# Kernel optimization log

Measured on AMD Instinct MI355X. Metric: run time of the kernel, lower is better.

Reference implementation:

```python
import jax, jax.numpy as jnp
import numpy as np

NINP, NHID, NOUT = 400, 600, 400
HS = NHID + NOUT          # h_size = nhid + nout
NLEVELS, K, AUX_FREQ = 40, 2, 20
DILATION = [1]


def setup_inputs() -> dict:
    key = jax.random.key(0)
    ks = jax.random.split(key, 6)
    B, T = 8, 256
    bound = 0.01  # matches init_weights normal_(0, 0.01)
    return {
        "X": jax.random.normal(ks[0], (B, NINP, T), jnp.float32),
        "hid": jax.random.normal(ks[1], (B, HS, 1), jnp.float32),
        "cell": jax.random.normal(ks[2], (B, HS, 1), jnp.float32),
        "w1": jax.random.normal(ks[3], (4 * HS, NINP, K), jnp.float32) * bound,
        "w2": jax.random.normal(ks[4], (4 * HS, HS, K), jnp.float32) * bound,
        "b2": jax.random.normal(ks[5], (4 * HS,), jnp.float32) * bound,
    }


def _conv1d(x, w, d):
    # x: [B, Cin, T_padded], w: [Cout, Cin, K] -> [B, Cout, T]
    return jax.lax.conv_general_dilated(
        x, w, window_strides=(1,), padding='VALID', rhs_dilation=(d,),
        dimension_numbers=('NCH', 'OIH', 'NCH'))


def _forward(X, hid, cell, w1, w2, b2):
    B, _, T = X.shape
    ht = jnp.zeros((B, HS, T), X.dtype)
    ct = jnp.zeros((B, HS, T), X.dtype)

    # Input-side convolution is weight-tied and X never changes across levels,
    # so (like the torch dict cache) compute it once per distinct dilation.
    conv1 = {}
    for d in set(DILATION):
        pad = (K - 1) * d
        xp = jnp.pad(X, ((0, 0), (0, 0), (pad, 0)))
        conv1[d] = _conv1d(xp, w1, d)

    aux = []
    for i in range(NLEVELS):
        d = DILATION[i % len(DILATION)]
        pad = (K - 1) * d
        # causal left-pad of the hidden stream, filled with the initial hid
        z1 = jnp.concatenate([jnp.broadcast_to(hid, (B, HS, pad)), ht], axis=2)
        out = conv1[d] + _conv1d(z1, w2, d) + b2[None, :, None]  # [B, 4*HS, T]
        # shifted cell state, first d steps filled with the initial cell
        ct_1 = jnp.concatenate(
            [jnp.broadcast_to(cell, (B, HS, d)), ct[:, :, :-d]], axis=2)
        it = jax.nn.sigmoid(out[:, :HS])
        ot = jax.nn.sigmoid(out[:, HS:2 * HS])
        gt = jnp.tanh(out[:, 2 * HS:3 * HS])
        ft = jax.nn.sigmoid(out[:, 3 * HS:])
        ct = ft * ct_1 + it * gt
        ht = ot * jnp.tanh(ct)
        if i % AUX_FREQ == AUX_FREQ - 1:
            aux.append(ht[:, -NOUT:])  # [B, nout, T]

    out_main = jnp.transpose(ht[:, -NOUT:], (0, 2, 1))            # [B, T, nout]
    hc = (ht[:, :, -1:], ct[:, :, -1:])                            # ([B,HS,1], [B,HS,1])
    aux_outs = jnp.transpose(jnp.stack(aux, axis=0), (1, 0, 3, 2))  # [B, n_aux, T, nout]
    return out_main, hc, aux_outs


def reference(X, hid, cell, w1, w2, b2):
    return _forward(X, hid, cell, w1, w2, b2)
```

## Files before the change

### kernel.cpp

```cpp
#include <hip/hip_runtime.h>
#include <hip/hip_bf16.h>
#include <math.h>

typedef __bf16 bf16;
typedef __bf16 bf16x8 __attribute__((ext_vector_type(8)));
typedef __bf16 bf16x4 __attribute__((ext_vector_type(4)));
typedef float f32x4 __attribute__((ext_vector_type(4)));
typedef float f32x16 __attribute__((ext_vector_type(16)));
typedef unsigned int u32;
typedef u32 u32x4 __attribute__((ext_vector_type(4)));

#define NINP 400
#define HS   1000
#define HP   1024
#define B_   8
#define T_   256
#define NT   2048
#define K2   2048
#define K1   1024
#define M_   4096

#define HT_OFF   819200
#define CT_OFF   827200
#define AUX_OFF  835200

typedef __attribute__((address_space(1))) const void gvoid;
typedef __attribute__((address_space(3))) void lvoid;

__device__ __forceinline__ void async_copy16(void* lds, const void* g) {
  __builtin_amdgcn_global_load_lds((gvoid*)g, (lvoid*)lds, 16, 0, 0);
}

__device__ __forceinline__ float sigm(float x) { return 1.0f / (1.0f + expf(-x)); }


__global__ void repack_w1(const float* __restrict__ w1, bf16* __restrict__ W1q) {
  int idx = blockIdx.x * 256 + threadIdx.x;
  if (idx >= M_ * K1) return;
  int m = idx >> 10, k = idx & 1023;
  int g = (m >> 3) & 3, h = (m >> 5) * 8 + (m & 7);
  float v = 0.0f;
  if (h < HS) {
    int c = g * HS + h;
    if (k < 512) { if (k < NINP) v = w1[(size_t)c * (NINP * 2) + k * 2 + 0]; }
    else { int j = k - 512; if (j < NINP) v = w1[(size_t)c * (NINP * 2) + j * 2 + 1]; }
  }
  W1q[idx] = (bf16)v;
}

__global__ void repack_w2(const float* __restrict__ w2, bf16* __restrict__ W2q) {
  int idx = blockIdx.x * 256 + threadIdx.x;
  if (idx >= M_ * K2) return;
  int m = idx >> 11, k = idx & 2047;
  int g = (m >> 3) & 3, h = (m >> 5) * 8 + (m & 7);
  float v = 0.0f;
  if (h < HS) {
    int c = g * HS + h;
    if (k < HP) { if (k < HS) v = w2[(size_t)c * (HS * 2) + k * 2 + 0]; }
    else { int j = k - HP; if (j < HS) v = w2[(size_t)c * (HS * 2) + j * 2 + 1]; }
  }
  W2q[idx] = (bf16)v;
}

__global__ void build_xt(const float* __restrict__ X, bf16* __restrict__ XT) {
  int idx = blockIdx.x * 256 + threadIdx.x;
  if (idx >= NT * K1) return;
  int n = idx >> 10, k = idx & 1023;
  int b = n >> 8, t = n & (T_ - 1);
  float v = 0.0f;
  if (k < 512) { if (k < NINP && t > 0) v = X[((size_t)b * NINP + k) * T_ + t - 1]; }
  else { int j = k - 512; if (j < NINP) v = X[((size_t)b * NINP + j) * T_ + t]; }
  XT[idx] = (bf16)v;
}

__global__ void build_hc(const float* __restrict__ hid, const float* __restrict__ cell,
                         bf16* __restrict__ hidp, float* __restrict__ cellp) {
  int idx = blockIdx.x * 256 + threadIdx.x;
  if (idx >= B_ * HP) return;
  int b = idx >> 10, k = idx & (HP - 1);
  hidp[idx]  = (k < HS) ? (bf16)hid[b * HS + k] : (bf16)0.0f;
  cellp[idx] = (k < HS) ? cell[b * HS + k] : 0.0f;
}


template <bool GATED>
__global__ __launch_bounds__(256, 2) void gemm_step(
    const bf16* __restrict__ A,
    const bf16* __restrict__ Bsrc,
    const bf16* __restrict__ hidp,
    const bf16* __restrict__ CbIn,
    bf16* __restrict__ CbOut,
    const float* __restrict__ b2,
    const bf16* __restrict__ ctprev,
    const float* __restrict__ cellp,
    bf16* __restrict__ ctnew,
    bf16* __restrict__ Hnew,
    int K) {
  __shared__ bf16 SMEM[2][128][64];

  const int tid = threadIdx.x;
  const int lane = tid & 63;
  const int w = tid >> 6;
  const int mh = w >> 1, nh = w & 1;
  const int dr = lane >> 3, c8 = lane & 7;
  const int swo = ((c8 - dr) & 7) * 8;
  const int row32 = lane & 31, q2 = lane >> 5;

  int n0, bm;
  if (GATED) {
    const int L = blockIdx.y * gridDim.x + blockIdx.x;
    bm = (L & 7) * 4 + (L >> 7);
    n0 = ((L >> 3) & 15) * 128;
  } else {
    n0 = blockIdx.x * 128;
    bm = blockIdx.y;
  }

  f32x16 acc[2][2];
#pragma unroll
  for (int i = 0; i < 2; ++i)
#pragma unroll
    for (int j = 0; j < 2; ++j)
#pragma unroll
      for (int e = 0; e < 16; ++e) acc[i][j][e] = 0.0f;

  bf16x4 cbr[2][2][4];
  if (GATED) {
#pragma unroll
    for (int mt = 0; mt < 2; ++mt) {
      const int tt = mh * 2 + mt;
#pragma unroll
      for (int nt = 0; nt < 2; ++nt) {
        const int n = n0 + nh * 64 + nt * 32 + row32;
        const size_t cb = (size_t)n * 4096 + (size_t)(bm * 4 + tt) * 32 + 4 * q2;
#pragma unroll
        for (int g = 0; g < 4; ++g)
          cbr[mt][nt][g] = *(const bf16x4*)&CbIn[cb + g * 8];
      }
    }
  }

  const int NIT = K >> 6;
  for (int it = 0; it < NIT; ++it) {
    const int k0 = it << 6;
    __syncthreads();
#pragma unroll
    for (int inst = 0; inst < 4; ++inst) {
      const int r = inst * 32 + w * 8 + dr;
      async_copy16(&SMEM[0][inst * 32 + w * 8][0],
                   A + (size_t)(bm * 128 + r) * K + k0 + swo);
      const int n = n0 + r;
      const bf16* bp;
      if (GATED) {
        const int kk = (k0 & (HP - 1)) + swo;
        if (k0 < HP) {
          const int t = n & (T_ - 1);
          bp = (t == 0) ? (hidp + (size_t)(n >> 8) * HP + kk)
                        : (Bsrc + (size_t)(n - 1) * HP + kk);
        } else {
          bp = Bsrc + (size_t)n * HP + kk;
        }
      } else {
        bp = Bsrc + (size_t)n * K + k0 + swo;
      }
      async_copy16(&SMEM[1][inst * 32 + w * 8][0], bp);
    }
    __syncthreads();
#pragma unroll
    for (int kc = 0; kc < 4; ++kc) {
      const int l = kc * 2 + q2;
      bf16x8 av[2], bv[2];
#pragma unroll
      for (int mt = 0; mt < 2; ++mt) {
        const int r = mh * 64 + mt * 32 + row32;
        av[mt] = *(const bf16x8*)&SMEM[0][r][((l + r) & 7) * 8];
      }
#pragma unroll
      for (int nt = 0; nt < 2; ++nt) {
        const int r = nh * 64 + nt * 32 + row32;
        bv[nt] = *(const bf16x8*)&SMEM[1][r][((l + r) & 7) * 8];
      }
#pragma unroll
      for (int mt = 0; mt < 2; ++mt)
#pragma unroll
        for (int nt = 0; nt < 2; ++nt)
          acc[mt][nt] = __builtin_amdgcn_mfma_f32_32x32x16_bf16(av[mt], bv[nt], acc[mt][nt], 0, 0, 0);
    }
  }

  if (!GATED) {
    __syncthreads();
    bf16 (*Csh)[128] = (bf16(*)[128])&SMEM[0][0][0];
#pragma unroll
    for (int mt = 0; mt < 2; ++mt) {
      const int tt = mh * 2 + mt;
#pragma unroll
      for (int nt = 0; nt < 2; ++nt) {
        const int nloc = nh * 64 + nt * 32 + row32;
#pragma unroll
        for (int g = 0; g < 4; ++g) {
          bf16x4 v;
#pragma unroll
          for (int j = 0; j < 4; ++j) {
            const int h = bm * 32 + tt * 8 + 4 * q2 + j;
            const float bias = (h < HS) ? b2[g * HS + h] : 0.0f;
            v[j] = (bf16)(acc[mt][nt][g * 4 + j] + bias);
          }
          *(bf16x4*)&Csh[nloc][tt * 32 + g * 8 + 4 * q2] = v;
        }
      }
    }
    __syncthreads();
#pragma unroll
    for (int i2 = 0; i2 < 8; ++i2) {
      const int idx = i2 * 256 + tid;
      const int rrow = idx >> 4, off = idx & 15;
      *(u32x4*)&CbOut[(size_t)(n0 + rrow) * 4096 + bm * 128 + off * 8] =
          *(const u32x4*)&Csh[rrow][off * 8];
    }
  } else {
    __syncthreads();
    bf16 (*Hsh)[32] = (bf16(*)[32])&SMEM[0][0][0];
#pragma unroll
    for (int mt = 0; mt < 2; ++mt) {
      const int tt = mh * 2 + mt;
#pragma unroll
      for (int nt = 0; nt < 2; ++nt) {
        const int nloc = nh * 64 + nt * 32 + row32;
        const int n = n0 + nloc;
        const int b = n >> 8;
        const int t = n & (T_ - 1);
        bf16x4 hv;
#pragma unroll
        for (int j = 0; j < 4; ++j) {
          const int h = bm * 32 + tt * 8 + 4 * q2 + j;
          const float ci = acc[mt][nt][0 + j]  + (float)cbr[mt][nt][0][j];
          const float co = acc[mt][nt][4 + j]  + (float)cbr[mt][nt][1][j];
          const float cg = acc[mt][nt][8 + j]  + (float)cbr[mt][nt][2][j];
          const float cf = acc[mt][nt][12 + j] + (float)cbr[mt][nt][3][j];
          const float ctold = (t == 0) ? cellp[b * HP + h]
                                       : (float)ctprev[(size_t)h * NT + (n - 1)];
          const float cn = sigm(cf) * ctold + sigm(ci) * tanhf(cg);
          ctnew[(size_t)h * NT + n] = (bf16)cn;
          hv[j] = (bf16)(sigm(co) * tanhf(cn));
        }
        *(bf16x4*)&Hsh[nloc][tt * 8 + 4 * q2] = hv;
      }
    }
    __syncthreads();
#pragma unroll
    for (int i2 = 0; i2 < 2; ++i2) {
      const int idx = i2 * 256 + tid;
      const int rrow = idx >> 2, off = idx & 3;
      *(u32x4*)&Hnew[(size_t)(n0 + rrow) * HP + bm * 32 + off * 8] =
          *(const u32x4*)&Hsh[rrow][off * 8];
    }
  }
}


__global__ void aux_kernel(const bf16* __restrict__ H, float* __restrict__ out, int s) {
  int idx = blockIdx.x * 256 + threadIdx.x;
  if (idx >= NT * 100) return;
  int n = idx / 100;
  int o = (idx % 100) * 4;
  int b = n >> 8, t = n & (T_ - 1);
  bf16x4 v = *(const bf16x4*)&H[(size_t)n * HP + 600 + o];
  f32x4 f = {(float)v[0], (float)v[1], (float)v[2], (float)v[3]};
  *(f32x4*)&out[AUX_OFF + ((size_t)((b * 2 + s) * T_ + t)) * 400 + o] = f;
}

__global__ void final_kernel(const bf16* __restrict__ H, const bf16* __restrict__ ct,
                             float* __restrict__ out) {
  int idx = blockIdx.x * 256 + threadIdx.x;
  if (idx < NT * 100) {
    int n = idx / 100;
    int o = (idx % 100) * 4;
    int b = n >> 8, t = n & (T_ - 1);
    bf16x4 v = *(const bf16x4*)&H[(size_t)n * HP + 600 + o];
    f32x4 f = {(float)v[0], (float)v[1], (float)v[2], (float)v[3]};
    *(f32x4*)&out[(size_t)n * 400 + o] = f;
    *(f32x4*)&out[AUX_OFF + ((size_t)((b * 2 + 1) * T_ + t)) * 400 + o] = f;
  } else {
    int j = idx - NT * 100;
    if (j < 8000) {
      int b = j / 1000, h = j % 1000;
      out[HT_OFF + j] = (float)H[(size_t)(b * T_ + 255) * HP + h];
    } else if (j < 16000) {
      int jj = j - 8000;
      int b = jj / 1000, h = jj % 1000;
      out[CT_OFF + jj] = (float)ct[(size_t)h * NT + b * T_ + 255];
    }
  }
}


extern "C" void kernel_launch(void* const* d_in, const int* in_sizes, int n_in,
                              void* d_out, int out_size, void* d_ws, size_t ws_size,
                              hipStream_t stream) {
  const float* X    = (const float*)d_in[0];
  const float* hid  = (const float*)d_in[1];
  const float* cell = (const float*)d_in[2];
  const float* w1   = (const float*)d_in[3];
  const float* w2   = (const float*)d_in[4];
  const float* b2   = (const float*)d_in[5];
  float* out = (float*)d_out;

  char* ws = (char*)d_ws;
  size_t off = 0;
  auto alloc = [&](size_t bytes) {
    void* p = ws + off;
    off += (bytes + 255) & ~(size_t)255;
    return p;
  };
  bf16* W2q    = (bf16*)alloc((size_t)M_ * K2 * 2);
  bf16* CbP    = (bf16*)alloc((size_t)NT * M_ * 2);
  bf16* Hb0    = (bf16*)alloc((size_t)NT * HP * 2);
  bf16* ctb0   = (bf16*)alloc((size_t)HP * NT * 2);
  bf16* hidp   = (bf16*)alloc((size_t)B_ * HP * 2);
  float* cellp = (float*)alloc((size_t)B_ * HP * 4);
  char* R = (char*)alloc((size_t)12 * 1024 * 1024);
  bf16* W1q  = (bf16*)R;
  bf16* XT   = (bf16*)(R + (size_t)8 * 1024 * 1024);
  bf16* ctb1 = (bf16*)R;
  bf16* Hb1  = (bf16*)(R + (size_t)4 * 1024 * 1024);

  bf16* Hb[2]  = {Hb0, Hb1};
  bf16* ctb[2] = {ctb0, ctb1};

  hipMemsetAsync(Hb[0], 0, (size_t)NT * HP * 2, stream);
  hipMemsetAsync(ctb[0], 0, (size_t)HP * NT * 2, stream);

  repack_w1<<<(M_ * K1) / 256, 256, 0, stream>>>(w1, W1q);
  repack_w2<<<(M_ * K2) / 256, 256, 0, stream>>>(w2, W2q);
  build_xt<<<(NT * K1) / 256, 256, 0, stream>>>(X, XT);
  build_hc<<<(B_ * HP) / 256, 256, 0, stream>>>(hid, cell, hidp, cellp);

  dim3 grid(NT / 128, M_ / 128);
  gemm_step<false><<<grid, 256, 0, stream>>>(W1q, XT, nullptr, nullptr, CbP, b2,
                                             nullptr, nullptr, nullptr, nullptr, K1);
  for (int i = 0; i < 40; ++i) {
    int p = i & 1;
    gemm_step<true><<<grid, 256, 0, stream>>>(W2q, Hb[p], hidp, CbP, nullptr, nullptr,
                                              ctb[p], cellp, ctb[p ^ 1], Hb[p ^ 1], K2);
    if (i == 19) aux_kernel<<<800, 256, 0, stream>>>(Hb[p ^ 1], out, 0);
  }
  final_kernel<<<(NT * 100 + 16000 + 255) / 256, 256, 0, stream>>>(Hb[0], ctb[0], out);
}
```

Before: 2.423 ms.

## Switch GEMM to 16x16x32 MFMA tiles with matching gate-interleaved weight layout

Replaces the 32x32x16 bf16 MFMA with 16x16x32 MFMA using a 4x4 per-wave accumulator grid, and changes the weight repacking so each 16-row M tile holds a single gate. This lets each lane see all four gates for the same hidden unit directly in acc[g][nt]. The gated epilogue now loads the precomputed input-conv values after the main loop instead of holding them in registers across it, which lowers register pressure. The tradeoff is different LDS read patterns and MFMA issue behaviour, with a risk of added bank conflicts or lower MFMA throughput.

```diff
diff --git a/kernel.cpp b/kernel.cpp
--- a/kernel.cpp
+++ b/kernel.cpp
@@ -6,7 +6,6 @@
 typedef __bf16 bf16x8 __attribute__((ext_vector_type(8)));
 typedef __bf16 bf16x4 __attribute__((ext_vector_type(4)));
 typedef float f32x4 __attribute__((ext_vector_type(4)));
-typedef float f32x16 __attribute__((ext_vector_type(16)));
 typedef unsigned int u32;
 typedef u32 u32x4 __attribute__((ext_vector_type(4)));
 
@@ -37,8 +36,9 @@
 __global__ void repack_w1(const float* __restrict__ w1, bf16* __restrict__ W1q) {
   int idx = blockIdx.x * 256 + threadIdx.x;
   if (idx >= M_ * K1) return;
-  int m = idx >> 10, k = idx & 1023;
-  int g = (m >> 3) & 3, h = (m >> 5) * 8 + (m & 7);
+  int pm = idx >> 10, k = idx & 1023;
+  int g = (pm >> 4) & 3;
+  int h = (pm >> 7) * 32 + ((pm >> 6) & 1) * 16 + (pm & 15);
   float v = 0.0f;
   if (h < HS) {
     int c = g * HS + h;
@@ -51,8 +51,9 @@
 __global__ void repack_w2(const float* __restrict__ w2, bf16* __restrict__ W2q) {
   int idx = blockIdx.x * 256 + threadIdx.x;
   if (idx >= M_ * K2) return;
-  int m = idx >> 11, k = idx & 2047;
-  int g = (m >> 3) & 3, h = (m >> 5) * 8 + (m & 7);
+  int pm = idx >> 11, k = idx & 2047;
+  int g = (pm >> 4) & 3;
+  int h = (pm >> 7) * 32 + ((pm >> 6) & 1) * 16 + (pm & 15);
   float v = 0.0f;
   if (h < HS) {
     int c = g * HS + h;
@@ -104,7 +105,7 @@
   const int mh = w >> 1, nh = w & 1;
   const int dr = lane >> 3, c8 = lane & 7;
   const int swo = ((c8 - dr) & 7) * 8;
-  const int row32 = lane & 31, q2 = lane >> 5;
+  const int quad = lane >> 4, col = lane & 15;
 
   int n0, bm;
   if (GATED) {
@@ -116,29 +117,11 @@
     bm = blockIdx.y;
   }
 
-  f32x16 acc[2][2];
-#pragma unroll
-  for (int i = 0; i < 2; ++i)
-#pragma unroll
-    for (int j = 0; j < 2; ++j)
-#pragma unroll
-      for (int e = 0; e < 16; ++e) acc[i][j][e] = 0.0f;
-
-  bf16x4 cbr[2][2][4];
-  if (GATED) {
-#pragma unroll
-    for (int mt = 0; mt < 2; ++mt) {
-      const int tt = mh * 2 + mt;
-#pragma unroll
-      for (int nt = 0; nt < 2; ++nt) {
-        const int n = n0 + nh * 64 + nt * 32 + row32;
-        const size_t cb = (size_t)n * 4096 + (size_t)(bm * 4 + tt) * 32 + 4 * q2;
-#pragma unroll
-        for (int g = 0; g < 4; ++g)
-          cbr[mt][nt][g] = *(const bf16x4*)&CbIn[cb + g * 8];
-      }
-    }
-  }
+  f32x4 acc[4][4];
+#pragma unroll
+  for (int i = 0; i < 4; ++i)
+#pragma unroll
+    for (int j = 0; j < 4; ++j) acc[i][j] = (f32x4){0.f, 0.f, 0.f, 0.f};
 
   const int NIT = K >> 6;
   for (int it = 0; it < NIT; ++it) {
@@ -167,24 +150,23 @@
     }
     __syncthreads();
 #pragma unroll
-    for (int kc = 0; kc < 4; ++kc) {
-      const int l = kc * 2 + q2;
-      bf16x8 av[2], bv[2];
-#pragma unroll
-      for (int mt = 0; mt < 2; ++mt) {
-        const int r = mh * 64 + mt * 32 + row32;
-        av[mt] = *(const bf16x8*)&SMEM[0][r][((l + r) & 7) * 8];
-      }
-#pragma unroll
-      for (int nt = 0; nt < 2; ++nt) {
-        const int r = nh * 64 + nt * 32 + row32;
-        bv[nt] = *(const bf16x8*)&SMEM[1][r][((l + r) & 7) * 8];
-      }
-#pragma unroll
-      for (int mt = 0; mt < 2; ++mt)
-#pragma unroll
-        for (int nt = 0; nt < 2; ++nt)
-          acc[mt][nt] = __builtin_amdgcn_mfma_f32_32x32x16_bf16(av[mt], bv[nt], acc[mt][nt], 0, 0, 0);
+    for (int kc = 0; kc < 64; kc += 32) {
+      bf16x8 av[4], bv[4];
+#pragma unroll
+      for (int mt = 0; mt < 4; ++mt) {
+        const int rA = mh * 64 + mt * 16 + col;
+        av[mt] = *(const bf16x8*)&SMEM[0][rA][(((kc >> 3) + quad + rA) & 7) * 8];
+      }
+#pragma unroll
+      for (int nt = 0; nt < 4; ++nt) {
+        const int rB = nh * 64 + nt * 16 + col;
+        bv[nt] = *(const bf16x8*)&SMEM[1][rB][(((kc >> 3) + quad + rB) & 7) * 8];
+      }
+#pragma unroll
+      for (int mt = 0; mt < 4; ++mt)
+#pragma unroll
+        for (int nt = 0; nt < 4; ++nt)
+          acc[mt][nt] = __builtin_amdgcn_mfma_f32_16x16x32_bf16(av[mt], bv[nt], acc[mt][nt], 0, 0, 0);
     }
   }
 
@@ -192,22 +174,18 @@
     __syncthreads();
     bf16 (*Csh)[128] = (bf16(*)[128])&SMEM[0][0][0];
 #pragma unroll
-    for (int mt = 0; mt < 2; ++mt) {
-      const int tt = mh * 2 + mt;
-#pragma unroll
-      for (int nt = 0; nt < 2; ++nt) {
-        const int nloc = nh * 64 + nt * 32 + row32;
-#pragma unroll
-        for (int g = 0; g < 4; ++g) {
-          bf16x4 v;
-#pragma unroll
-          for (int j = 0; j < 4; ++j) {
-            const int h = bm * 32 + tt * 8 + 4 * q2 + j;
-            const float bias = (h < HS) ? b2[g * HS + h] : 0.0f;
-            v[j] = (bf16)(acc[mt][nt][g * 4 + j] + bias);
-          }
-          *(bf16x4*)&Csh[nloc][tt * 32 + g * 8 + 4 * q2] = v;
+    for (int mt = 0; mt < 4; ++mt) {
+#pragma unroll
+      for (int nt = 0; nt < 4; ++nt) {
+        const int nloc = nh * 64 + nt * 16 + col;
+        bf16x4 v;
+#pragma unroll
+        for (int j = 0; j < 4; ++j) {
+          const int h = bm * 32 + mh * 16 + quad * 4 + j;
+          const float bias = (h < HS) ? b2[mt * HS + h] : 0.0f;
+          v[j] = (bf16)(acc[mt][nt][j] + bias);
         }
+        *(bf16x4*)&Csh[nloc][mh * 64 + mt * 16 + quad * 4] = v;
       }
     }
     __syncthreads();
@@ -222,30 +200,31 @@
     __syncthreads();
     bf16 (*Hsh)[32] = (bf16(*)[32])&SMEM[0][0][0];
 #pragma unroll
-    for (int mt = 0; mt < 2; ++mt) {
-      const int tt = mh * 2 + mt;
-#pragma unroll
-      for (int nt = 0; nt < 2; ++nt) {
-        const int nloc = nh * 64 + nt * 32 + row32;
-        const int n = n0 + nloc;
-        const int b = n >> 8;
-        const int t = n & (T_ - 1);
-        bf16x4 hv;
-#pragma unroll
-        for (int j = 0; j < 4; ++j) {
-          const int h = bm * 32 + tt * 8 + 4 * q2 + j;
-          const float ci = acc[mt][nt][0 + j]  + (float)cbr[mt][nt][0][j];
-          const float co = acc[mt][nt][4 + j]  + (float)cbr[mt][nt][1][j];
-          const float cg = acc[mt][nt][8 + j]  + (float)cbr[mt][nt][2][j];
-          const float cf = acc[mt][nt][12 + j] + (float)cbr[mt][nt][3][j];
-          const float ctold = (t == 0) ? cellp[b * HP + h]
-                                       : (float)ctprev[(size_t)h * NT + (n - 1)];
-          const float cn = sigm(cf) * ctold + sigm(ci) * tanhf(cg);
-          ctnew[(size_t)h * NT + n] = (bf16)cn;
-          hv[j] = (bf16)(sigm(co) * tanhf(cn));
-        }
-        *(bf16x4*)&Hsh[nloc][tt * 8 + 4 * q2] = hv;
-      }
+    for (int nt = 0; nt < 4; ++nt) {
+      const int nloc = nh * 64 + nt * 16 + col;
+      const int n = n0 + nloc;
+      const int b = n >> 8;
+      const int t = n & (T_ - 1);
+      const size_t cb = (size_t)n * 4096 + (size_t)(bm * 2 + mh) * 64 + quad * 4;
+      bf16x4 c0 = *(const bf16x4*)&CbIn[cb + 0];
+      bf16x4 c1 = *(const bf16x4*)&CbIn[cb + 16];
+      bf16x4 c2 = *(const bf16x4*)&CbIn[cb + 32];
+      bf16x4 c3 = *(const bf16x4*)&CbIn[cb + 48];
+      bf16x4 hv;
+#pragma unroll
+      for (int j = 0; j < 4; ++j) {
+        const int h = bm * 32 + mh * 16 + quad * 4 + j;
+        const float ci = acc[0][nt][j] + (float)c0[j];
+        const float co = acc[1][nt][j] + (float)c1[j];
+        const float cg = acc[2][nt][j] + (float)c2[j];
+        const float cf = acc[3][nt][j] + (float)c3[j];
+        const float ctold = (t == 0) ? cellp[b * HP + h]
+                                     : (float)ctprev[(size_t)h * NT + (n - 1)];
+        const float cn = sigm(cf) * ctold + sigm(ci) * tanhf(cg);
+        ctnew[(size_t)h * NT + n] = (bf16)cn;
+        hv[j] = (bf16)(sigm(co) * tanhf(cn));
+      }
+      *(bf16x4*)&Hsh[nloc][mh * 16 + quad * 4] = hv;
     }
     __syncthreads();
 #pragma unroll
```

Measured after the change: 1.999 ms. 17.5% less time.
